# Performance work log

Measured on AMD Instinct MI355X. Metric: run time of the kernel, lower is better.

## Reference

```python
import jax, jax.numpy as jnp
import numpy as np

N, INPUT_DIM, HIDDEN_DIM, REL_DIM, OUT_DIM = 512, 128, 256, 128, 64


def setup_inputs() -> dict:
    key = jax.random.key(0)
    ks = jax.random.split(key, 9)
    s = lambda fan_in: 1.0 / np.sqrt(fan_in)
    return {
        "node_feats": jax.random.normal(ks[0], (N, INPUT_DIM), dtype=jnp.float32),
        "W1": jax.random.uniform(ks[1], (2 * INPUT_DIM, HIDDEN_DIM), minval=-s(2 * INPUT_DIM), maxval=s(2 * INPUT_DIM), dtype=jnp.float32),
        "b1": jax.random.uniform(ks[2], (HIDDEN_DIM,), minval=-s(2 * INPUT_DIM), maxval=s(2 * INPUT_DIM), dtype=jnp.float32),
        "W2": jax.random.uniform(ks[3], (HIDDEN_DIM, REL_DIM), minval=-s(HIDDEN_DIM), maxval=s(HIDDEN_DIM), dtype=jnp.float32),
        "b2": jax.random.uniform(ks[4], (REL_DIM,), minval=-s(HIDDEN_DIM), maxval=s(HIDDEN_DIM), dtype=jnp.float32),
        "W3": jax.random.uniform(ks[5], (REL_DIM, 64), minval=-s(REL_DIM), maxval=s(REL_DIM), dtype=jnp.float32),
        "b3": jax.random.uniform(ks[6], (64,), minval=-s(REL_DIM), maxval=s(REL_DIM), dtype=jnp.float32),
        "W4": jax.random.uniform(ks[7], (64, OUT_DIM), minval=-s(64), maxval=s(64), dtype=jnp.float32),
        "b4": jax.random.uniform(ks[8], (OUT_DIM,), minval=-s(64), maxval=s(64), dtype=jnp.float32),
    }


def reference(node_feats, W1, b1, W2, b2, W3, b3, W4, b4):
    n, d = node_feats.shape
    # Pairwise concat: pair[i, j] = [node_feats[i], node_feats[j]]  -> [N*N, 2d]
    left = jnp.broadcast_to(node_feats[:, None, :], (n, n, d))
    right = jnp.broadcast_to(node_feats[None, :, :], (n, n, d))
    pairs = jnp.concatenate([left, right], axis=-1).reshape(n * n, 2 * d)
    h = jax.nn.relu(pairs @ W1 + b1)            # [N^2, hidden]
    r = jax.nn.relu(h @ W2 + b2)                # [N^2, rel]
    R = jnp.mean(r, axis=0)                     # [rel]
    out = jax.nn.relu(R @ W3 + b3) @ W4 + b4    # [out_dim]
    return out
```

## Files before the change

kernel.cpp:

```cpp
#include <hip/hip_runtime.h>
#include <hip/hip_fp16.h>

#define NN   512
#define D    128
#define HID  256
#define REL  128
#define ODIM 64
#define NBLK 2048

typedef __attribute__((ext_vector_type(4))) float        f32x4;
typedef __attribute__((ext_vector_type(8))) _Float16     f16x8;
typedef __attribute__((ext_vector_type(4))) unsigned int u32x4;

union H8 { u32x4 u4; f16x8 h8; unsigned int u[4]; };

__global__ void kAW(const float* __restrict__ X, const float* __restrict__ W1,
                    const float* __restrict__ b1, _Float16* __restrict__ Aph,
                    _Float16* __restrict__ Bh,
                    const float* __restrict__ W2, _Float16* __restrict__ W2f) {
    __shared__ float Xs[4][D];
    int t = threadIdx.x;
    if (blockIdx.x >= 128) {
        int gid = (blockIdx.x - 128) * 256 + t;
        int s  = gid >> 9;
        int cf = (gid >> 6) & 7;
        int l  = gid & 63;
        int kb = s * 32 + 8 * (l >> 4);
        int c  = cf * 16 + (l & 15);
        H8 pkd;
#pragma unroll
        for (int e = 0; e < 8; ++e) pkd.h8[e] = (_Float16)W2[(kb + e) * REL + c];
        *(u32x4*)&W2f[(size_t)gid * 8] = pkd.u4;
        return;
    }
    int r0 = blockIdx.x * 4;
#pragma unroll
    for (int q = 0; q < 2; ++q) {
        int idx = q * 256 + t;
        Xs[idx >> 7][idx & 127] = X[(r0 + (idx >> 7)) * D + (idx & 127)];
    }
    __syncthreads();
    float a[4], b[4];
    float b1c = b1[t];
#pragma unroll
    for (int r = 0; r < 4; ++r) { a[r] = b1c; b[r] = 0.f; }
#pragma unroll 4
    for (int k = 0; k < D; ++k) {
        float wt = W1[k * HID + t];
        float wb = W1[(D + k) * HID + t];
#pragma unroll
        for (int r = 0; r < 4; ++r) {
            a[r] += Xs[r][k] * wt;
            b[r] += Xs[r][k] * wb;
        }
    }
#pragma unroll
    for (int r = 0; r < 4; ++r) {
        Aph[(r0 + r) * HID + t] = (_Float16)a[r];
        Bh[(r0 + r) * HID + t]  = (_Float16)b[r];
    }
}

__global__ __launch_bounds__(256, 3) void kB(const _Float16* __restrict__ Aph,
                                             const _Float16* __restrict__ Bh,
                                             const _Float16* __restrict__ W2f,
                                             const float* __restrict__ b2,
                                             float* __restrict__ partial) {
    __shared__ _Float16 Ash[8][264];
    __shared__ _Float16 Bsh[16][264];

    int t   = threadIdx.x;
    int w   = t >> 6;
    int l   = t & 63;
    int blk = blockIdx.x;
    int i0  = (blk >> 5) * 8;
    int j0  = (blk & 31) * 16;
    int c0  = w * 32;
    int kg  = l >> 4;
    int jl  = l & 15;

    H8 w2r[16];
#pragma unroll
    for (int s = 0; s < 8; ++s)
#pragma unroll
        for (int n = 0; n < 2; ++n)
            w2r[2 * s + n].u4 = *(const u32x4*)&W2f[(size_t)((s * 8 + (w * 2 + n)) * 64 + l) * 8];

    {
        int r = t >> 5, c8 = t & 31;
        *(u32x4*)&Ash[r][c8 * 8] = *(const u32x4*)&Aph[(i0 + r) * HID + c8 * 8];
    }
#pragma unroll
    for (int q = 0; q < 2; ++q) {
        int idx = q * 256 + t;
        int r = idx >> 5, c8 = idx & 31;
        *(u32x4*)&Bsh[r][c8 * 8] = *(const u32x4*)&Bh[(j0 + r) * HID + c8 * 8];
    }
    __syncthreads();

    H8 brow[8];
#pragma unroll
    for (int s = 0; s < 8; ++s) brow[s].u4 = *(const u32x4*)&Bsh[jl][s * 32 + kg * 8];

    f32x4 acc[8][2];
#pragma unroll
    for (int pf = 0; pf < 8; ++pf)
#pragma unroll
        for (int n = 0; n < 2; ++n) acc[pf][n] = (f32x4){0.f, 0.f, 0.f, 0.f};

    const f16x8 zero8 = (f16x8)(_Float16)0.f;

    H8 ac[8], an[8];
#pragma unroll
    for (int pf = 0; pf < 8; ++pf)
        ac[pf] = *(const H8*)&Ash[pf][kg * 8];

#pragma unroll
    for (int s = 0; s < 8; ++s) {
        if (s < 7) {
#pragma unroll
            for (int pf = 0; pf < 8; ++pf)
                an[pf] = *(const H8*)&Ash[pf][(s + 1) * 32 + kg * 8];
        }
#pragma unroll
        for (int pf = 0; pf < 8; ++pf) {
            f16x8 sum = ac[pf].h8 + brow[s].h8;
            H8 af;
            af.h8 = __builtin_elementwise_max(sum, zero8);
            acc[pf][0] = __builtin_amdgcn_mfma_f32_16x16x32_f16(af.h8, w2r[2 * s + 0].h8, acc[pf][0], 0, 0, 0);
            acc[pf][1] = __builtin_amdgcn_mfma_f32_16x16x32_f16(af.h8, w2r[2 * s + 1].h8, acc[pf][1], 0, 0, 0);
        }
#pragma unroll
        for (int pf = 0; pf < 8; ++pf) ac[pf] = an[pf];
    }

    float b2v0 = b2[c0 + jl];
    float b2v1 = b2[c0 + 16 + jl];
    float s0 = 0.f, s1 = 0.f;
#pragma unroll
    for (int pf = 0; pf < 8; ++pf)
#pragma unroll
        for (int r = 0; r < 4; ++r) {
            s0 += fmaxf(acc[pf][0][r] + b2v0, 0.f);
            s1 += fmaxf(acc[pf][1][r] + b2v1, 0.f);
        }
    s0 += __shfl_xor(s0, 16); s0 += __shfl_xor(s0, 32);
    s1 += __shfl_xor(s1, 16); s1 += __shfl_xor(s1, 32);
    if (l < 16) {
        partial[blk * REL + c0 + l]      = s0;
        partial[blk * REL + c0 + 16 + l] = s1;
    }
}

__global__ void kR(const float* __restrict__ partial, float* __restrict__ R) {
    int o = blockIdx.x;
    int t = threadIdx.x;
    float s = 0.f;
    for (int b = t; b < NBLK; b += 256) s += partial[b * REL + o];
    __shared__ float sh[256];
    sh[t] = s;
    __syncthreads();
    for (int st = 128; st > 0; st >>= 1) {
        if (t < st) sh[t] += sh[t + st];
        __syncthreads();
    }
    if (t == 0) R[o] = sh[0] * (1.f / 262144.f);
}

__global__ void kC(const float* __restrict__ R, const float* __restrict__ W3,
                   const float* __restrict__ b3, const float* __restrict__ W4,
                   const float* __restrict__ b4, float* __restrict__ out) {
    __shared__ float Rsh[REL];
    __shared__ float t1[ODIM];
    int t = threadIdx.x;
    Rsh[t] = R[t];
    __syncthreads();
    if (t < ODIM) {
        float s = b3[t];
#pragma unroll 8
        for (int k = 0; k < REL; ++k) s += Rsh[k] * W3[k * ODIM + t];
        t1[t] = fmaxf(s, 0.f);
    }
    __syncthreads();
    if (t < ODIM) {
        float s = b4[t];
#pragma unroll 8
        for (int k = 0; k < ODIM; ++k) s += t1[k] * W4[k * ODIM + t];
        out[t] = s;
    }
}

extern "C" void kernel_launch(void* const* d_in, const int* in_sizes, int n_in,
                              void* d_out, int out_size, void* d_ws, size_t ws_size,
                              hipStream_t stream) {
    const float* X  = (const float*)d_in[0];
    const float* W1 = (const float*)d_in[1];
    const float* b1 = (const float*)d_in[2];
    const float* W2 = (const float*)d_in[3];
    const float* b2 = (const float*)d_in[4];
    const float* W3 = (const float*)d_in[5];
    const float* b3 = (const float*)d_in[6];
    const float* W4 = (const float*)d_in[7];
    const float* b4 = (const float*)d_in[8];
    float* out = (float*)d_out;

    char* ws = (char*)d_ws;
    _Float16* Aph     = (_Float16*)ws;
    _Float16* Bh      = (_Float16*)(ws + 262144);
    _Float16* W2f     = (_Float16*)(ws + 524288);
    float*    partial = (float*)(ws + 589824);
    float*    R       = (float*)(ws + 1638400);

    kAW<<<144, 256, 0, stream>>>(X, W1, b1, Aph, Bh, W2, W2f);
    kB<<<NBLK, 256, 0, stream>>>(Aph, Bh, W2f, b2, partial);
    kR<<<REL, 256, 0, stream>>>(partial, R);
    kC<<<1, 128, 0, stream>>>(R, W3, b3, W4, b4, out);
}
```

Before: 40.93 us.

## Restructure pair-MLP kernel into persistent double-buffered tiles with 32x32 MFMA

The main kernel now runs 512 persistent blocks. Each block loops over 8 tile pairs and uses global_load_lds to double-buffer the A and B rows into shared memory, overlapping loads with compute. It switches from 16x16x32 to 32x32x16 MFMA and splits the output channels across block pairs, keeping W2 fragments resident in registers. B and W2 are pre-laid out in kAW to match the fragment order. The final reduction becomes a single small block. Register pressure goes up, with launch bounds lowered to 2 blocks per SM.

```diff
diff --git a/kernel.cpp b/kernel.cpp
--- a/kernel.cpp
+++ b/kernel.cpp
@@ -6,33 +6,42 @@
 #define HID  256
 #define REL  128
 #define ODIM 64
-#define NBLK 2048
-
-typedef __attribute__((ext_vector_type(4))) float        f32x4;
-typedef __attribute__((ext_vector_type(8))) _Float16     f16x8;
-typedef __attribute__((ext_vector_type(4))) unsigned int u32x4;
-
-union H8 { u32x4 u4; f16x8 h8; unsigned int u[4]; };
+
+typedef __attribute__((ext_vector_type(4)))  float        f32x4;
+typedef __attribute__((ext_vector_type(16))) float        f32x16;
+typedef __attribute__((ext_vector_type(8)))  _Float16     f16x8;
+typedef __attribute__((ext_vector_type(4)))  unsigned int u32x4;
+
+union H8 { u32x4 u4; f16x8 h8; };
+
+#define WAIT_VM(N) asm volatile("s_waitcnt vmcnt(" #N ")" ::: "memory")
+#define BARRIER()  do { asm volatile("" ::: "memory"); __builtin_amdgcn_s_barrier(); asm volatile("" ::: "memory"); } while (0)
+
+__device__ __forceinline__ void cp16(void* l, const void* g) {
+    __builtin_amdgcn_global_load_lds((const __attribute__((address_space(1))) unsigned int*)g,
+                                     (__attribute__((address_space(3))) unsigned int*)l, 16, 0, 0);
+}
 
 __global__ void kAW(const float* __restrict__ X, const float* __restrict__ W1,
                     const float* __restrict__ b1, _Float16* __restrict__ Aph,
-                    _Float16* __restrict__ Bh,
-                    const float* __restrict__ W2, _Float16* __restrict__ W2f) {
-    __shared__ float Xs[4][D];
+                    _Float16* __restrict__ Bg,
+                    const float* __restrict__ W2, _Float16* __restrict__ W2g) {
     int t = threadIdx.x;
     if (blockIdx.x >= 128) {
         int gid = (blockIdx.x - 128) * 256 + t;
-        int s  = gid >> 9;
-        int cf = (gid >> 6) & 7;
-        int l  = gid & 63;
-        int kb = s * 32 + 8 * (l >> 4);
-        int c  = cf * 16 + (l & 15);
+        int f = gid >> 6, l = gid & 63;
+        int cg = f >> 4, ks = f & 15;
         H8 pkd;
 #pragma unroll
-        for (int e = 0; e < 8; ++e) pkd.h8[e] = (_Float16)W2[(kb + e) * REL + c];
-        *(u32x4*)&W2f[(size_t)gid * 8] = pkd.u4;
+        for (int e = 0; e < 8; ++e) {
+            int k = ks * 16 + (l >> 5) * 8 + e;
+            int c = cg * 32 + (l & 31);
+            pkd.h8[e] = (_Float16)W2[k * REL + c];
+        }
+        *(u32x4*)&W2g[(size_t)gid * 8] = pkd.u4;
         return;
     }
+    __shared__ float Xs[4][D];
     int r0 = blockIdx.x * 4;
 #pragma unroll
     for (int q = 0; q < 2; ++q) {
@@ -54,117 +63,122 @@
             b[r] += Xs[r][k] * wb;
         }
     }
+    int ks = t >> 4, hs = (t >> 3) & 1, e = t & 7;
 #pragma unroll
     for (int r = 0; r < 4; ++r) {
-        Aph[(r0 + r) * HID + t] = (_Float16)a[r];
-        Bh[(r0 + r) * HID + t]  = (_Float16)b[r];
-    }
-}
-
-__global__ __launch_bounds__(256, 3) void kB(const _Float16* __restrict__ Aph,
-                                             const _Float16* __restrict__ Bh,
-                                             const _Float16* __restrict__ W2f,
+        int row = r0 + r;
+        Aph[row * HID + t] = (_Float16)a[r];
+        Bg[(row >> 4) * 4096 + ks * 256 + hs * 128 + (row & 15) * 8 + e] = (_Float16)b[r];
+    }
+}
+
+__global__ __launch_bounds__(256, 2) void kB(const _Float16* __restrict__ Aph,
+                                             const _Float16* __restrict__ Bg,
+                                             const _Float16* __restrict__ W2g,
                                              const float* __restrict__ b2,
                                              float* __restrict__ partial) {
-    __shared__ _Float16 Ash[8][264];
-    __shared__ _Float16 Bsh[16][264];
-
-    int t   = threadIdx.x;
-    int w   = t >> 6;
-    int l   = t & 63;
+    __shared__ __align__(16) char smem[2][12288];
+    __shared__ float redsh[4][2][32];
+
+    int t = threadIdx.x, w = t >> 6, l = t & 63;
     int blk = blockIdx.x;
-    int i0  = (blk >> 5) * 8;
-    int j0  = (blk & 31) * 16;
-    int c0  = w * 32;
-    int kg  = l >> 4;
-    int jl  = l & 15;
-
-    H8 w2r[16];
-#pragma unroll
-    for (int s = 0; s < 8; ++s)
-#pragma unroll
-        for (int n = 0; n < 2; ++n)
-            w2r[2 * s + n].u4 = *(const u32x4*)&W2f[(size_t)((s * 8 + (w * 2 + n)) * 64 + l) * 8];
+    int ch = blk & 1, tg = blk >> 1;
+    int l31 = l & 31, hs = l >> 5, j = l & 15;
+    int i_loc = (w << 1) + (l31 >> 4);
+
+    H8 w2r[2][16];
+#pragma unroll
+    for (int cgi = 0; cgi < 2; ++cgi)
+#pragma unroll
+        for (int ks = 0; ks < 16; ++ks)
+            w2r[cgi][ks].u4 = *(const u32x4*)&W2g[(size_t)((((ch * 2 + cgi) * 16 + ks) * 64) + l) * 8];
+
+    float b2c0 = b2[ch * 64 + l31];
+    float b2c1 = b2[ch * 64 + 32 + l31];
+
+    const f16x8 zero8 = (f16x8)(_Float16)0.f;
+    float psum0 = 0.f, psum1 = 0.f;
 
     {
-        int r = t >> 5, c8 = t & 31;
-        *(u32x4*)&Ash[r][c8 * 8] = *(const u32x4*)&Aph[(i0 + r) * HID + c8 * 8];
-    }
-#pragma unroll
-    for (int q = 0; q < 2; ++q) {
-        int idx = q * 256 + t;
-        int r = idx >> 5, c8 = idx & 31;
-        *(u32x4*)&Bsh[r][c8 * 8] = *(const u32x4*)&Bh[(j0 + r) * HID + c8 * 8];
-    }
-    __syncthreads();
-
-    H8 brow[8];
-#pragma unroll
-    for (int s = 0; s < 8; ++s) brow[s].u4 = *(const u32x4*)&Bsh[jl][s * 32 + kg * 8];
-
-    f32x4 acc[8][2];
-#pragma unroll
-    for (int pf = 0; pf < 8; ++pf)
-#pragma unroll
-        for (int n = 0; n < 2; ++n) acc[pf][n] = (f32x4){0.f, 0.f, 0.f, 0.f};
-
-    const f16x8 zero8 = (f16x8)(_Float16)0.f;
-
-    H8 ac[8], an[8];
-#pragma unroll
-    for (int pf = 0; pf < 8; ++pf)
-        ac[pf] = *(const H8*)&Ash[pf][kg * 8];
-
-#pragma unroll
-    for (int s = 0; s < 8; ++s) {
-        if (s < 7) {
-#pragma unroll
-            for (int pf = 0; pf < 8; ++pf)
-                an[pf] = *(const H8*)&Ash[pf][(s + 1) * 32 + kg * 8];
-        }
-#pragma unroll
-        for (int pf = 0; pf < 8; ++pf) {
-            f16x8 sum = ac[pf].h8 + brow[s].h8;
-            H8 af;
-            af.h8 = __builtin_elementwise_max(sum, zero8);
-            acc[pf][0] = __builtin_amdgcn_mfma_f32_16x16x32_f16(af.h8, w2r[2 * s + 0].h8, acc[pf][0], 0, 0, 0);
-            acc[pf][1] = __builtin_amdgcn_mfma_f32_16x16x32_f16(af.h8, w2r[2 * s + 1].h8, acc[pf][1], 0, 0, 0);
-        }
-#pragma unroll
-        for (int pf = 0; pf < 8; ++pf) ac[pf] = an[pf];
-    }
-
-    float b2v0 = b2[c0 + jl];
-    float b2v1 = b2[c0 + 16 + jl];
-    float s0 = 0.f, s1 = 0.f;
-#pragma unroll
-    for (int pf = 0; pf < 8; ++pf)
-#pragma unroll
-        for (int r = 0; r < 4; ++r) {
-            s0 += fmaxf(acc[pf][0][r] + b2v0, 0.f);
-            s1 += fmaxf(acc[pf][1][r] + b2v1, 0.f);
-        }
-    s0 += __shfl_xor(s0, 16); s0 += __shfl_xor(s0, 32);
-    s1 += __shfl_xor(s1, 16); s1 += __shfl_xor(s1, 32);
-    if (l < 16) {
-        partial[blk * REL + c0 + l]      = s0;
-        partial[blk * REL + c0 + 16 + l] = s1;
+        int tau = tg;
+        int i0 = (tau >> 5) * 8, jt = tau & 31;
+        cp16(&smem[0][w * 1024 + l * 16], &Aph[(i0 + 2 * w + hs) * HID + l31 * 8]);
+        cp16(&smem[0][4096 + (2 * w) * 1024 + l * 16],
+             (const char*)Bg + jt * 8192 + (2 * w) * 1024 + l * 16);
+        cp16(&smem[0][4096 + (2 * w + 1) * 1024 + l * 16],
+             (const char*)Bg + jt * 8192 + (2 * w + 1) * 1024 + l * 16);
+    }
+
+#pragma unroll 1
+    for (int u = 0; u < 8; ++u) {
+        int cur = u & 1;
+        if (u < 7) {
+            int tau = tg + (u + 1) * 256;
+            int i0 = (tau >> 5) * 8, jt = tau & 31;
+            int nb = cur ^ 1;
+            cp16(&smem[nb][w * 1024 + l * 16], &Aph[(i0 + 2 * w + hs) * HID + l31 * 8]);
+            cp16(&smem[nb][4096 + (2 * w) * 1024 + l * 16],
+                 (const char*)Bg + jt * 8192 + (2 * w) * 1024 + l * 16);
+            cp16(&smem[nb][4096 + (2 * w + 1) * 1024 + l * 16],
+                 (const char*)Bg + jt * 8192 + (2 * w + 1) * 1024 + l * 16);
+            WAIT_VM(3);
+        } else {
+            WAIT_VM(0);
+        }
+        BARRIER();
+
+        const char* base  = &smem[cur][0];
+        const char* abase = base + i_loc * 512 + hs * 16;
+        const char* bbase = base + 4096 + hs * 256 + j * 16;
+
+        f32x16 acc0, acc1;
+#pragma unroll
+        for (int r = 0; r < 16; ++r) { acc0[r] = 0.f; acc1[r] = 0.f; }
+
+#pragma unroll
+        for (int ks = 0; ks < 16; ++ks) {
+            H8 a = *(const H8*)(abase + ks * 32);
+            H8 b = *(const H8*)(bbase + ks * 512);
+            f16x8 sum = a.h8 + b.h8;
+            H8 h; h.h8 = __builtin_elementwise_max(sum, zero8);
+            acc0 = __builtin_amdgcn_mfma_f32_32x32x16_f16(h.h8, w2r[0][ks].h8, acc0, 0, 0, 0);
+            acc1 = __builtin_amdgcn_mfma_f32_32x32x16_f16(h.h8, w2r[1][ks].h8, acc1, 0, 0, 0);
+        }
+
+        float s0 = 0.f, s1 = 0.f;
+#pragma unroll
+        for (int r = 0; r < 16; ++r) {
+            s0 += fmaxf(acc0[r] + b2c0, 0.f);
+            s1 += fmaxf(acc1[r] + b2c1, 0.f);
+        }
+        psum0 += s0; psum1 += s1;
+        BARRIER();
+    }
+
+    psum0 += __shfl_xor(psum0, 32);
+    psum1 += __shfl_xor(psum1, 32);
+    if (l < 32) { redsh[w][0][l] = psum0; redsh[w][1][l] = psum1; }
+    __syncthreads();
+    if (w == 0 && l < 32) {
+        float t0 = redsh[0][0][l] + redsh[1][0][l] + redsh[2][0][l] + redsh[3][0][l];
+        float t1 = redsh[0][1][l] + redsh[1][1][l] + redsh[2][1][l] + redsh[3][1][l];
+        partial[blk * 64 + l]      = t0;
+        partial[blk * 64 + 32 + l] = t1;
     }
 }
 
 __global__ void kR(const float* __restrict__ partial, float* __restrict__ R) {
-    int o = blockIdx.x;
+    __shared__ float sh[256];
     int t = threadIdx.x;
+    int c = t & 127, g = t >> 7;
+    int ch = c >> 6, cc = c & 63;
     float s = 0.f;
-    for (int b = t; b < NBLK; b += 256) s += partial[b * REL + o];
-    __shared__ float sh[256];
+#pragma unroll 4
+    for (int k = g * 128; k < g * 128 + 128; ++k)
+        s += partial[(2 * k + ch) * 64 + cc];
     sh[t] = s;
     __syncthreads();
-    for (int st = 128; st > 0; st >>= 1) {
-        if (t < st) sh[t] += sh[t + st];
-        __syncthreads();
-    }
-    if (t == 0) R[o] = sh[0] * (1.f / 262144.f);
+    if (t < 128) R[t] = (sh[t] + sh[t + 128]) * (1.f / 262144.f);
 }
 
 __global__ void kC(const float* __restrict__ R, const float* __restrict__ W3,
@@ -206,13 +220,13 @@
 
     char* ws = (char*)d_ws;
     _Float16* Aph     = (_Float16*)ws;
-    _Float16* Bh      = (_Float16*)(ws + 262144);
-    _Float16* W2f     = (_Float16*)(ws + 524288);
+    _Float16* Bg      = (_Float16*)(ws + 262144);
+    _Float16* W2g     = (_Float16*)(ws + 524288);
     float*    partial = (float*)(ws + 589824);
-    float*    R       = (float*)(ws + 1638400);
-
-    kAW<<<144, 256, 0, stream>>>(X, W1, b1, Aph, Bh, W2, W2f);
-    kB<<<NBLK, 256, 0, stream>>>(Aph, Bh, W2f, b2, partial);
-    kR<<<REL, 256, 0, stream>>>(partial, R);
+    float*    R       = (float*)(ws + 720896);
+
+    kAW<<<144, 256, 0, stream>>>(X, W1, b1, Aph, Bg, W2, W2g);
+    kB<<<512, 256, 0, stream>>>(Aph, Bg, W2g, b2, partial);
+    kR<<<1, 256, 0, stream>>>(partial, R);
     kC<<<1, 128, 0, stream>>>(R, W3, b3, W4, b4, out);
 }
```

Measured after the change: 43.92 us. +7.3%, slower.
